# Performance work log

Hardware: AMD Instinct MI355X
Metric: run time of the kernel (lower is better)

Reference implementation:

```python
import jax, jax.numpy as jnp
import numpy as np

E = 128       # embed_size
H = 256       # hidden_size
Q = 256       # query_size
B = 256       # batch size
N_ENT = 200000
N_REL = 500
N_NODES = 100000   # existing (head) nodes
N_NEW = 50000      # new tail nodes (segment_sum size)
M = 200000         # edges


def setup_inputs() -> dict:
    key = jax.random.key(0)
    ks = jax.random.split(key, 32)
    s = 0.02
    inp = {
        'entity_emb':   jax.random.normal(ks[0], (N_ENT, E), jnp.float32),
        'relation_emb': jax.random.normal(ks[1], (N_REL, E), jnp.float32),
        'node_hidden':  jax.random.normal(ks[2], (N_NODES, H), jnp.float32),
        'query_repr':   jax.random.normal(ks[3], (B, Q), jnp.float32),
        # attention params (Ws_attn, Wr_attn, Wqr_attn, w_alpha)
        'Ws':  jax.random.normal(ks[4], (H, H), jnp.float32) * s,
        'Wr':  jax.random.normal(ks[5], (E, H), jnp.float32) * s,
        'Wqr': jax.random.normal(ks[6], (E, H), jnp.float32) * s,
        'bqr': jnp.zeros((H,), jnp.float32),
        'w_alpha': jax.random.normal(ks[7], (H, 1), jnp.float32) * s,
        'b_alpha': jnp.zeros((1,), jnp.float32),
        # GRUCell (input = 2E message, hidden = H), torch layout [3H, in]
        'W_ih': jax.random.normal(ks[8], (3 * H, 2 * E), jnp.float32) * s,
        'W_hh': jax.random.normal(ks[9], (3 * H, H), jnp.float32) * s,
        'b_ih': jnp.zeros((3 * H,), jnp.float32),
        'b_hh': jnp.zeros((3 * H,), jnp.float32),
        # We2h: entity embed -> initial hidden
        'We2h_W': jax.random.normal(ks[10], (E, H), jnp.float32) * s,
        'We2h_b': jnp.zeros((H,), jnp.float32),
        # candidate_layer: [2E + H] -> H (agent_num = 1)
        'cand_W': jax.random.normal(ks[11], (2 * E + H, H), jnp.float32) * s,
        'cand_b': jnp.zeros((H,), jnp.float32),
        # rank_layer: [H + Q] -> 1
        'rank_W': jax.random.normal(ks[12], (H + Q, 1), jnp.float32) * s,
        'rank_b': jnp.zeros((1,), jnp.float32),
        # LayerNorm
        'ln_g': jnp.ones((H,), jnp.float32),
        'ln_b': jnp.zeros((H,), jnp.float32),
        # edge list (int constants)
        'head_node':     jax.random.randint(ks[13], (M,), 0, N_NODES, jnp.int32),
        'edge_rel':      jax.random.randint(ks[14], (M,), 0, N_REL, jnp.int32),
        'tail_ent':      jax.random.randint(ks[15], (M,), 0, N_ENT, jnp.int32),
        'tail_node':     jax.random.randint(ks[16], (M,), 0, N_NEW, jnp.int32),
        'query_rel':     jax.random.randint(ks[17], (M,), 0, N_REL, jnp.int32),
        'batch_idx':     jax.random.randint(ks[18], (M,), 0, B, jnp.int32),
        'tail_node_ent': jax.random.randint(ks[19], (N_NEW,), 0, N_ENT, jnp.int32),
    }
    return inp


def reference(entity_emb, relation_emb, node_hidden, query_repr,
              Ws, Wr, Wqr, bqr, w_alpha, b_alpha,
              W_ih, W_hh, b_ih, b_hh, We2h_W, We2h_b,
              cand_W, cand_b, rank_W, rank_b, ln_g, ln_b,
              head_node, edge_rel, tail_ent, tail_node, query_rel,
              batch_idx, tail_node_ent):
    lrelu = lambda x: jax.nn.leaky_relu(x, 0.01)
    # --- per-edge attention: w_alpha(ReLU(Ws h_s + Wr h_r + Wqr h_q)) ---
    hs = node_hidden[head_node]            # [M, H]
    hr = relation_emb[edge_rel]            # [M, E]
    hq = relation_emb[query_rel]           # [M, E]
    attn_feat = jax.nn.relu(hs @ Ws + hr @ Wr + hq @ Wqr + bqr)   # [M, H]
    alpha = jax.nn.sigmoid(attn_feat @ w_alpha + b_alpha)         # [M, 1]
    # --- attention-weighted message (rel || tail entity) scattered to tails ---
    te = entity_emb[tail_ent]                                     # [M, E]
    msg = jnp.concatenate([hr, te], axis=-1) * alpha              # [M, 2E]
    agg = jax.ops.segment_sum(msg, tail_node, num_segments=N_NEW) # [N_NEW, 2E]
    # --- GRUCell update of tail-node hidden states ---
    h_prev = lrelu(entity_emb[tail_node_ent] @ We2h_W + We2h_b)   # [N_NEW, H]
    gx = agg @ W_ih.T + b_ih                                      # [N_NEW, 3H]
    gh = h_prev @ W_hh.T + b_hh
    xr, xz, xn = jnp.split(gx, 3, axis=-1)
    hr_, hz_, hn_ = jnp.split(gh, 3, axis=-1)
    r = jax.nn.sigmoid(xr + hr_)
    z = jax.nn.sigmoid(xz + hz_)
    n = jnp.tanh(xn + r * hn_)
    h_new = (1.0 - z) * n + z * h_prev                            # [N_NEW, H]
    mu = jnp.mean(h_new, axis=-1, keepdims=True)
    var = jnp.var(h_new, axis=-1, keepdims=True)
    h_new = (h_new - mu) * jax.lax.rsqrt(var + 1e-5) * ln_g + ln_b
    # --- candidate scoring: candidate_layer + rank_layer ---
    cand_in = jnp.concatenate([te, hr, h_new[tail_node]], axis=-1)   # [M, 2E+H]
    cand_h = lrelu(cand_in @ cand_W + cand_b)                        # [M, H]
    rank_in = jnp.concatenate([cand_h, query_repr[batch_idx]], -1)   # [M, H+Q]
    scores = (rank_in @ rank_W + rank_b)[:, 0]                       # [M]
    return scores
```

## Files before the change

### kernel.cpp

```cpp
#include <hip/hip_runtime.h>
#include <math.h>


#define ACT_NONE 0
#define ACT_LRELU 1

typedef __attribute__((ext_vector_type(8))) short short8;
typedef __attribute__((ext_vector_type(4))) float floatx4;

__device__ __forceinline__ ushort f2b(float x) {
    union { float f; unsigned u; } v; v.f = x;
    return (ushort)((v.u + 0x7fffu + ((v.u >> 16) & 1u)) >> 16);
}
__device__ __forceinline__ float b2f(ushort b) {
    union { unsigned u; float f; } v; v.u = ((unsigned)b) << 16;
    return v.f;
}
__device__ __forceinline__ void gload16(const ushort* g, ushort* l) {
    __builtin_amdgcn_global_load_lds(
        (const __attribute__((address_space(1))) void*)g,
        (__attribute__((address_space(3))) void*)l, 16, 0, 0);
}

__global__ __launch_bounds__(256) void gemm_k(
    const float* __restrict__ A, const float* __restrict__ B,
    const float* __restrict__ bias, float* __restrict__ C,
    int M, int N, int K, const int* __restrict__ a_idx, int act)
{
    __shared__ float As[16][68];
    __shared__ float Bs[16][68];
    const int tid = threadIdx.x;
    const int tx = tid & 15, ty = tid >> 4;
    const int m0 = blockIdx.x * 64, n0 = blockIdx.y * 64;
    float acc[4][4] = {};
    const int ar  = tid >> 2;
    const int ac4 = (tid & 3) * 4;
    const int brow = tid >> 4;
    const int bc4  = (tid & 15) * 4;
    const int gm = m0 + ar;
    const float* Arow = nullptr;
    if (gm < M) {
        int r = a_idx ? a_idx[gm] : gm;
        Arow = A + (size_t)r * K;
    }
    for (int k0 = 0; k0 < K; k0 += 16) {
        float4 av = make_float4(0.f, 0.f, 0.f, 0.f);
        if (Arow) av = *(const float4*)(Arow + k0 + ac4);
        As[ac4 + 0][ar] = av.x;
        As[ac4 + 1][ar] = av.y;
        As[ac4 + 2][ar] = av.z;
        As[ac4 + 3][ar] = av.w;
        float4 bv = *(const float4*)(B + (size_t)(k0 + brow) * N + n0 + bc4);
        *(float4*)&Bs[brow][bc4] = bv;
        __syncthreads();
        #pragma unroll
        for (int kk = 0; kk < 16; ++kk) {
            float4 a4 = *(float4*)&As[kk][ty << 2];
            float4 b4 = *(float4*)&Bs[kk][tx << 2];
            float avr[4] = {a4.x, a4.y, a4.z, a4.w};
            float bvr[4] = {b4.x, b4.y, b4.z, b4.w};
            #pragma unroll
            for (int i = 0; i < 4; ++i)
                #pragma unroll
                for (int j = 0; j < 4; ++j)
                    acc[i][j] = fmaf(avr[i], bvr[j], acc[i][j]);
        }
        __syncthreads();
    }
    const int n = n0 + (tx << 2);
    float4 bv4 = make_float4(0.f, 0.f, 0.f, 0.f);
    if (bias) bv4 = *(const float4*)(bias + n);
    #pragma unroll
    for (int i = 0; i < 4; ++i) {
        int m = m0 + (ty << 2) + i;
        if (m >= M) continue;
        float v0 = acc[i][0] + bv4.x;
        float v1 = acc[i][1] + bv4.y;
        float v2 = acc[i][2] + bv4.z;
        float v3 = acc[i][3] + bv4.w;
        if (act == ACT_LRELU) {
            v0 = v0 > 0.f ? v0 : 0.01f * v0;
            v1 = v1 > 0.f ? v1 : 0.01f * v1;
            v2 = v2 > 0.f ? v2 : 0.01f * v2;
            v3 = v3 > 0.f ? v3 : 0.01f * v3;
        }
        *(float4*)(C + (size_t)m * N + n) = make_float4(v0, v1, v2, v3);
    }
}

__global__ __launch_bounds__(256) void convert16_k(
    const float* __restrict__ in, ushort* __restrict__ out, int n)
{
    int i = blockIdx.x * 256 + threadIdx.x;
    if (i < n) out[i] = f2b(in[i]);
}
__global__ __launch_bounds__(256) void transpose16_k(
    const float* __restrict__ in, ushort* __restrict__ out, int k0, int KS, int N)
{
    int i = blockIdx.x * 256 + threadIdx.x;
    if (i >= KS * N) return;
    int k = i / N, n = i - k * N;
    out[(size_t)n * KS + k] = f2b(in[(size_t)(k0 + k) * N + n]);
}

__global__ __launch_bounds__(256) void gemm16p_k(
    const ushort* __restrict__ A16, const int* __restrict__ a_idx,
    const ushort* __restrict__ BT, const float* __restrict__ bias,
    float* __restrict__ C, ushort* __restrict__ C16,
    int M, int N, int K, int act)
{
    __shared__ ushort As[2][128 * 32];
    __shared__ ushort Bs[2][128 * 32];
    const int tid = threadIdx.x;
    const int l = tid & 63, w = tid >> 6;
    const int m0 = blockIdx.y * 128, n0 = blockIdx.x * 128;

    const ushort* agp[2];
    const ushort* bgp[2];
    #pragma unroll
    for (int j = 0; j < 2; ++j) {
        int row = j * 64 + w * 16 + (l >> 2);
        int seg = (l & 3) ^ (row & 3);
        int r = m0 + row; if (r >= M) r = M - 1;
        int rr = a_idx ? a_idx[r] : r;
        agp[j] = A16 + (size_t)rr * K + seg * 8;
        bgp[j] = BT + (size_t)(n0 + row) * K + seg * 8;
    }

    const int wm = (w & 1) * 64, wn = (w >> 1) * 64;
    const int cl = l & 15, q = l >> 4;
    const int sseg = (q ^ (cl & 3)) * 8;
    const int aoff = (wm + cl) * 32 + sseg;
    const int boff = (wn + cl) * 32 + sseg;

    floatx4 acc[4][4];
    #pragma unroll
    for (int mi = 0; mi < 4; ++mi)
        #pragma unroll
        for (int ni = 0; ni < 4; ++ni) acc[mi][ni] = 0.f;

    const int NT = K >> 5;
    #pragma unroll
    for (int j = 0; j < 2; ++j) {
        gload16(agp[j], &As[0][j * 2048 + w * 512]);
        gload16(bgp[j], &Bs[0][j * 2048 + w * 512]);
    }
    __syncthreads();

    int buf = 0;
    for (int t = 0; t < NT; ++t) {
        if (t + 1 < NT) {
            int k0 = (t + 1) * 32;
            #pragma unroll
            for (int j = 0; j < 2; ++j) {
                gload16(agp[j] + k0, &As[buf ^ 1][j * 2048 + w * 512]);
                gload16(bgp[j] + k0, &Bs[buf ^ 1][j * 2048 + w * 512]);
            }
        }
        short8 af[4], bf[4];
        #pragma unroll
        for (int mi = 0; mi < 4; ++mi) af[mi] = *(short8*)&As[buf][aoff + mi * 512];
        #pragma unroll
        for (int ni = 0; ni < 4; ++ni) bf[ni] = *(short8*)&Bs[buf][boff + ni * 512];
        #pragma unroll
        for (int mi = 0; mi < 4; ++mi)
            #pragma unroll
            for (int ni = 0; ni < 4; ++ni)
                acc[mi][ni] = __builtin_amdgcn_mfma_f32_16x16x32_bf16(
                    bf[ni], af[mi], acc[mi][ni], 0, 0, 0);
        __syncthreads();
        buf ^= 1;
    }

    #pragma unroll
    for (int mi = 0; mi < 4; ++mi) {
        int row = m0 + wm + mi * 16 + cl;
        if (row >= M) continue;
        #pragma unroll
        for (int ni = 0; ni < 4; ++ni) {
            int col = n0 + wn + ni * 16 + q * 4;
            float4 bv = bias ? *(const float4*)(bias + col)
                             : make_float4(0.f, 0.f, 0.f, 0.f);
            float v[4];
            #pragma unroll
            for (int r = 0; r < 4; ++r) {
                float x = acc[mi][ni][r] + ((const float*)&bv)[r];
                if (act == ACT_LRELU) x = x > 0.f ? x : 0.01f * x;
                v[r] = x;
            }
            if (C16) {
                ushort4 u;
                u.x = f2b(v[0]); u.y = f2b(v[1]); u.z = f2b(v[2]); u.w = f2b(v[3]);
                *(ushort4*)(C16 + (size_t)row * N + col) = u;
            }
            if (C) *(float4*)(C + (size_t)row * N + col) =
                       make_float4(v[0], v[1], v[2], v[3]);
        }
    }
}

__global__ __launch_bounds__(256) void gemm16pf_k(
    const float* __restrict__ A, const ushort* __restrict__ BT,
    const float* __restrict__ bias, ushort* __restrict__ C16,
    int M, int N, int K, int act)
{
    __shared__ ushort As[2][128 * 32];
    __shared__ ushort Bs[2][128 * 32];
    const int tid = threadIdx.x;
    const int l = tid & 63, w = tid >> 6;
    const int m0 = blockIdx.y * 128, n0 = blockIdx.x * 128;

    const int rowbase = tid >> 3, f4 = tid & 7;
    const float* arow[4];
    int awadr[4];
    #pragma unroll
    for (int i = 0; i < 4; ++i) {
        int row = rowbase + i * 32;
        int r = m0 + row; if (r >= M) r = M - 1;
        arow[i] = A + (size_t)r * K;
        awadr[i] = row * 32 + (((f4 >> 1) ^ (row & 3)) * 8) + (f4 & 1) * 4;
    }
    const ushort* bgp[2];
    #pragma unroll
    for (int j = 0; j < 2; ++j) {
        int row = j * 64 + w * 16 + (l >> 2);
        int seg = (l & 3) ^ (row & 3);
        bgp[j] = BT + (size_t)(n0 + row) * K + seg * 8;
    }

    const int wm = (w & 1) * 64, wn = (w >> 1) * 64;
    const int cl = l & 15, q = l >> 4;
    const int sseg = (q ^ (cl & 3)) * 8;
    const int aoff = (wm + cl) * 32 + sseg;
    const int boff = (wn + cl) * 32 + sseg;

    floatx4 acc[4][4];
    #pragma unroll
    for (int mi = 0; mi < 4; ++mi)
        #pragma unroll
        for (int ni = 0; ni < 4; ++ni) acc[mi][ni] = 0.f;

    const int NT = K >> 5;
    #pragma unroll
    for (int j = 0; j < 2; ++j) gload16(bgp[j], &Bs[0][j * 2048 + w * 512]);
    #pragma unroll
    for (int i = 0; i < 4; ++i) {
        float4 v = *(const float4*)(arow[i] + f4 * 4);
        ushort4 u; u.x = f2b(v.x); u.y = f2b(v.y); u.z = f2b(v.z); u.w = f2b(v.w);
        *(ushort4*)&As[0][awadr[i]] = u;
    }
    __syncthreads();

    int buf = 0;
    for (int t = 0; t < NT; ++t) {
        float4 av[4];
        if (t + 1 < NT) {
            int k0 = (t + 1) * 32;
            #pragma unroll
            for (int j = 0; j < 2; ++j)
                gload16(bgp[j] + k0, &Bs[buf ^ 1][j * 2048 + w * 512]);
            #pragma unroll
            for (int i = 0; i < 4; ++i)
                av[i] = *(const float4*)(arow[i] + k0 + f4 * 4);
        }
        short8 af[4], bf[4];
        #pragma unroll
        for (int mi = 0; mi < 4; ++mi) af[mi] = *(short8*)&As[buf][aoff + mi * 512];
        #pragma unroll
        for (int ni = 0; ni < 4; ++ni) bf[ni] = *(short8*)&Bs[buf][boff + ni * 512];
        #pragma unroll
        for (int mi = 0; mi < 4; ++mi)
            #pragma unroll
            for (int ni = 0; ni < 4; ++ni)
                acc[mi][ni] = __builtin_amdgcn_mfma_f32_16x16x32_bf16(
                    bf[ni], af[mi], acc[mi][ni], 0, 0, 0);
        if (t + 1 < NT) {
            #pragma unroll
            for (int i = 0; i < 4; ++i) {
                ushort4 u;
                u.x = f2b(av[i].x); u.y = f2b(av[i].y);
                u.z = f2b(av[i].z); u.w = f2b(av[i].w);
                *(ushort4*)&As[buf ^ 1][awadr[i]] = u;
            }
        }
        __syncthreads();
        buf ^= 1;
    }

    #pragma unroll
    for (int mi = 0; mi < 4; ++mi) {
        int row = m0 + wm + mi * 16 + cl;
        if (row >= M) continue;
        #pragma unroll
        for (int ni = 0; ni < 4; ++ni) {
            int col = n0 + wn + ni * 16 + q * 4;
            float4 bv = bias ? *(const float4*)(bias + col)
                             : make_float4(0.f, 0.f, 0.f, 0.f);
            ushort4 u;
            float x0 = acc[mi][ni][0] + bv.x;
            float x1 = acc[mi][ni][1] + bv.y;
            float x2 = acc[mi][ni][2] + bv.z;
            float x3 = acc[mi][ni][3] + bv.w;
            if (act == ACT_LRELU) {
                x0 = x0 > 0.f ? x0 : 0.01f * x0;
                x1 = x1 > 0.f ? x1 : 0.01f * x1;
                x2 = x2 > 0.f ? x2 : 0.01f * x2;
                x3 = x3 > 0.f ? x3 : 0.01f * x3;
            }
            u.x = f2b(x0); u.y = f2b(x1); u.z = f2b(x2); u.w = f2b(x3);
            *(ushort4*)(C16 + (size_t)row * N + col) = u;
        }
    }
}

__global__ __launch_bounds__(256) void qdot_k(
    const float* __restrict__ q, const float* __restrict__ rank_W,
    float* __restrict__ qdot)
{
    int b = blockIdx.x * 4 + (threadIdx.x >> 6);
    int l = threadIdx.x & 63;
    float s = 0.f;
    #pragma unroll
    for (int k = 0; k < 4; ++k) {
        int h = l + k * 64;
        s += q[(size_t)b * 256 + h] * rank_W[256 + h];
    }
    #pragma unroll
    for (int off = 32; off; off >>= 1) s += __shfl_xor(s, off, 64);
    if (l == 0) qdot[b] = s;
}

__global__ __launch_bounds__(256) void alpha_k(
    const ushort* __restrict__ nodeWs16, const float* __restrict__ relWr,
    const float* __restrict__ relWqr, const float* __restrict__ bqr,
    const float* __restrict__ w_alpha, const float* __restrict__ b_alpha_p,
    const int* __restrict__ hcsr_hn, const int* __restrict__ hcsr_er,
    const int* __restrict__ hcsr_qr, const int* __restrict__ hcsr_e,
    float* __restrict__ alpha_out)
{
    const int tid = threadIdx.x;
    const int e0 = blockIdx.x * 32;
    __shared__ int hn[32], er[32], qr[32], se[32];
    if (tid < 32) {
        int i = e0 + tid;
        hn[tid] = hcsr_hn[i]; er[tid] = hcsr_er[i];
        qr[tid] = hcsr_qr[i]; se[tid] = hcsr_e[i];
    }
    __syncthreads();
    const int tx = tid & 63, ty = tid >> 6;
    const int c = tx * 4;
    const float4 bq = *(const float4*)(bqr + c);
    const float4 wa = *(const float4*)(w_alpha + c);
    float part[8];
    #pragma unroll
    for (int i2 = 0; i2 < 8; ++i2) {
        int i = ty * 8 + i2;
        ushort4 a16 = *(const ushort4*)(nodeWs16 + (size_t)hn[i] * 256 + c);
        float4 b = *(const float4*)(relWr + (size_t)er[i] * 256 + c);
        float4 d = *(const float4*)(relWqr + (size_t)qr[i] * 256 + c);
        float x0 = fmaxf(b2f(a16.x) + b.x + d.x + bq.x, 0.f);
        float x1 = fmaxf(b2f(a16.y) + b.y + d.y + bq.y, 0.f);
        float x2 = fmaxf(b2f(a16.z) + b.z + d.z + bq.z, 0.f);
        float x3 = fmaxf(b2f(a16.w) + b.w + d.w + bq.w, 0.f);
        part[i2] = x0 * wa.x + x1 * wa.y + x2 * wa.z + x3 * wa.w;
    }
    #pragma unroll
    for (int off = 32; off; off >>= 1)
        #pragma unroll
        for (int i2 = 0; i2 < 8; ++i2)
            part[i2] += __shfl_xor(part[i2], off, 64);
    if (tx == 0) {
        float ba = b_alpha_p[0];
        #pragma unroll
        for (int i2 = 0; i2 < 8; ++i2)
            alpha_out[se[ty * 8 + i2]] = 1.f / (1.f + __expf(-(part[i2] + ba)));
    }
}

__global__ __launch_bounds__(256) void hist_k(
    const int* __restrict__ key, int* __restrict__ deg, int M)
{
    int e = blockIdx.x * 256 + threadIdx.x;
    if (e < M) atomicAdd(&deg[key[e]], 1);
}
__global__ __launch_bounds__(512) void scan1_k(
    const int* __restrict__ deg, int* __restrict__ partial, int N)
{
    __shared__ int sm[512];
    int i = blockIdx.x * 512 + threadIdx.x;
    sm[threadIdx.x] = (i < N) ? deg[i] : 0;
    __syncthreads();
    for (int off = 256; off; off >>= 1) {
        if (threadIdx.x < off) sm[threadIdx.x] += sm[threadIdx.x + off];
        __syncthreads();
    }
    if (threadIdx.x == 0) partial[blockIdx.x] = sm[0];
}
__global__ __launch_bounds__(256) void scan2_k(
    int* __restrict__ partial, int nPart, int* __restrict__ offsets, int N, int M)
{
    __shared__ int sm[256];
    int t = threadIdx.x;
    int v = (t < nPart) ? partial[t] : 0;
    sm[t] = v;
    __syncthreads();
    for (int off = 1; off < 256; off <<= 1) {
        int add = (t >= off) ? sm[t - off] : 0;
        __syncthreads();
        sm[t] += add;
        __syncthreads();
    }
    if (t < nPart) partial[t] = sm[t] - v;
    if (t == 0) offsets[N] = M;
}
__global__ __launch_bounds__(512) void scan3_k(
    const int* __restrict__ deg, const int* __restrict__ partial,
    int* __restrict__ offsets, int* __restrict__ cursor, int N)
{
    __shared__ int sm[512];
    int i = blockIdx.x * 512 + threadIdx.x;
    int t = threadIdx.x;
    int v = (i < N) ? deg[i] : 0;
    sm[t] = v;
    __syncthreads();
    for (int off = 1; off < 512; off <<= 1) {
        int add = (t >= off) ? sm[t - off] : 0;
        __syncthreads();
        sm[t] += add;
        __syncthreads();
    }
    if (i < N) {
        int excl = partial[blockIdx.x] + sm[t] - v;
        offsets[i] = excl;
        cursor[i] = excl;
    }
}
__global__ __launch_bounds__(256) void fill_k(
    const int* __restrict__ tail_node, const int* __restrict__ tail_ent,
    const int* __restrict__ edge_rel, const int* __restrict__ batch_idx,
    int* __restrict__ cursor, int* __restrict__ ce, int* __restrict__ cte,
    int* __restrict__ cer, int* __restrict__ ctn, int* __restrict__ cbi, int M)
{
    int e = blockIdx.x * 256 + threadIdx.x;
    if (e < M) {
        int tn = tail_node[e];
        int pos = atomicAdd(&cursor[tn], 1);
        ce[pos] = e; cte[pos] = tail_ent[e]; cer[pos] = edge_rel[e];
        ctn[pos] = tn; cbi[pos] = batch_idx[e];
    }
}
__global__ __launch_bounds__(256) void hfill_k(
    const int* __restrict__ head_node, const int* __restrict__ edge_rel,
    const int* __restrict__ query_rel, int* __restrict__ cursor,
    int* __restrict__ hhn, int* __restrict__ her, int* __restrict__ hqr,
    int* __restrict__ he, int M)
{
    int e = blockIdx.x * 256 + threadIdx.x;
    if (e < M) {
        int h = head_node[e];
        int pos = atomicAdd(&cursor[h], 1);
        hhn[pos] = h; her[pos] = edge_rel[e]; hqr[pos] = query_rel[e]; he[pos] = e;
    }
}

__global__ __launch_bounds__(256) void agg_csr_k(
    const float* __restrict__ relation_emb, const ushort* __restrict__ ent16,
    const float* __restrict__ alpha, const int* __restrict__ csr_e,
    const int* __restrict__ csr_er, const int* __restrict__ csr_te,
    const int* __restrict__ offsets, ushort* __restrict__ agg16)
{
    int node = blockIdx.x * 4 + (threadIdx.x >> 6);
    int lane = threadIdx.x & 63;
    int beg = offsets[node], end = offsets[node + 1];
    float4 acc = make_float4(0.f, 0.f, 0.f, 0.f);
    const int c = lane * 4;
    for (int j = beg; j < end; ++j) {
        float a = alpha[csr_e[j]];
        float4 v;
        if (lane < 32) {
            v = *(const float4*)(relation_emb + (size_t)csr_er[j] * 128 + c);
        } else {
            ushort4 u = *(const ushort4*)(ent16 + (size_t)csr_te[j] * 128 + (c - 128));
            v = make_float4(b2f(u.x), b2f(u.y), b2f(u.z), b2f(u.w));
        }
        acc.x += v.x * a; acc.y += v.y * a;
        acc.z += v.z * a; acc.w += v.w * a;
    }
    ushort4 o;
    o.x = f2b(acc.x); o.y = f2b(acc.y); o.z = f2b(acc.z); o.w = f2b(acc.w);
    *(ushort4*)(agg16 + (size_t)node * 256 + c) = o;
}

__global__ __launch_bounds__(256) void gru_ln_k(
    const ushort* __restrict__ gx, const ushort* __restrict__ gh,
    const ushort* __restrict__ h_prev, const float* __restrict__ ln_g,
    const float* __restrict__ ln_b, ushort* __restrict__ h_new16, int n0)
{
    int nl = blockIdx.x * 4 + (threadIdx.x >> 6);
    int lane = threadIdx.x & 63;
    int n = n0 + nl;
    const ushort* gxr = gx + (size_t)nl * 768;
    const ushort* ghr = gh + (size_t)nl * 768;
    const ushort* hpr = h_prev + (size_t)n * 256;
    float hv[4]; float s = 0.f, s2 = 0.f;
    #pragma unroll
    for (int q2 = 0; q2 < 4; ++q2) {
        int h = lane + q2 * 64;
        float xr = b2f(gxr[h]), xz = b2f(gxr[256 + h]), xn = b2f(gxr[512 + h]);
        float hr_ = b2f(ghr[h]), hn_ = b2f(ghr[512 + h]);
        float hz_ = b2f(ghr[256 + h]);
        float hp = b2f(hpr[h]);
        float r = 1.f / (1.f + __expf(-(xr + hr_)));
        float z = 1.f / (1.f + __expf(-(xz + hz_)));
        float nn = tanhf(xn + r * hn_);
        float v = (1.f - z) * nn + z * hp;
        hv[q2] = v; s += v; s2 += v * v;
    }
    #pragma unroll
    for (int off = 32; off; off >>= 1) {
        s  += __shfl_xor(s, off, 64);
        s2 += __shfl_xor(s2, off, 64);
    }
    float mean = s * (1.f / 256.f);
    float var  = s2 * (1.f / 256.f) - mean * mean;
    float rstd = rsqrtf(var + 1e-5f);
    ushort* outr = h_new16 + (size_t)n * 256;
    #pragma unroll
    for (int q2 = 0; q2 < 4; ++q2) {
        int h = lane + q2 * 64;
        outr[h] = f2b((hv[q2] - mean) * rstd * ln_g[h] + ln_b[h]);
    }
}

__global__ __launch_bounds__(256) void score_mfma_k(
    const ushort* __restrict__ ent16, const ushort* __restrict__ candW1T,
    const ushort* __restrict__ relCand16, const ushort* __restrict__ hnewCand16,
    const float* __restrict__ rank_W, const float* __restrict__ rank_b_p,
    const float* __restrict__ qdot,
    const int* __restrict__ csr_e, const int* __restrict__ csr_te,
    const int* __restrict__ csr_er, const int* __restrict__ csr_tn,
    const int* __restrict__ csr_bi, float* __restrict__ scores, int M)
{
    __shared__ ushort As[128 * 136];
    __shared__ int s_er[128], s_tn[128];
    __shared__ float s_part[4][128];
    const int tid = threadIdx.x;
    const int e0 = blockIdx.x * 128;
    int cnt = M - e0; if (cnt > 128) cnt = 128;

    if (tid < 128) {
        int idx = e0 + (tid < cnt ? tid : 0);
        s_er[tid] = csr_er[idx];
        s_tn[tid] = csr_tn[idx];
    }
    {
        int row = tid >> 1;
        int idx = e0 + (row < cnt ? row : 0);
        const ushort* ar = ent16 + (size_t)csr_te[idx] * 128;
        int s0 = (tid & 1) * 8;
        #pragma unroll
        for (int j = 0; j < 8; ++j) {
            int seg = s0 + j;
            int slot = seg ^ (row & 3);
            *(uint4*)&As[row * 136 + slot * 8] = *(const uint4*)(ar + seg * 8);
        }
    }
    __syncthreads();

    const int l = tid & 63, w = tid >> 6;
    const int cl = l & 15, q = l >> 4;

    float rowsum[8];
    #pragma unroll
    for (int mi = 0; mi < 8; ++mi) rowsum[mi] = 0.f;

    #pragma unroll
    for (int ch = 0; ch < 2; ++ch) {
        floatx4 acc[8][2];
        #pragma unroll
        for (int mi = 0; mi < 8; ++mi)
            #pragma unroll
            for (int ni = 0; ni < 2; ++ni) acc[mi][ni] = 0.f;

        const ushort* bb = candW1T + (size_t)(w * 64 + ch * 32 + cl) * 128 + q * 8;
        #pragma unroll
        for (int k0 = 0; k0 < 128; k0 += 32) {
            short8 bf[2];
            #pragma unroll
            for (int ni = 0; ni < 2; ++ni)
                bf[ni] = *(const short8*)(bb + ni * 2048 + k0);
            #pragma unroll
            for (int mi = 0; mi < 8; ++mi) {
                int row = mi * 16 + cl;
                int slot = (((k0 >> 3) + q) ^ (cl & 3));
                short8 af = *(short8*)&As[row * 136 + slot * 8];
                #pragma unroll
                for (int ni = 0; ni < 2; ++ni)
                    acc[mi][ni] = __builtin_amdgcn_mfma_f32_16x16x32_bf16(
                        bf[ni], af, acc[mi][ni], 0, 0, 0);
            }
        }
        #pragma unroll
        for (int mi = 0; mi < 8; ++mi) {
            int row = mi * 16 + cl;
            int er = s_er[row], tn = s_tn[row];
            #pragma unroll
            for (int ni = 0; ni < 2; ++ni) {
                int col = w * 64 + ch * 32 + ni * 16 + q * 4;
                ushort4 rc = *(const ushort4*)(relCand16 + (size_t)er * 256 + col);
                ushort4 hc = *(const ushort4*)(hnewCand16 + (size_t)tn * 256 + col);
                float4 rw = *(const float4*)(rank_W + col);
                float v0 = acc[mi][ni][0] + b2f(rc.x) + b2f(hc.x);
                float v1 = acc[mi][ni][1] + b2f(rc.y) + b2f(hc.y);
                float v2 = acc[mi][ni][2] + b2f(rc.z) + b2f(hc.z);
                float v3 = acc[mi][ni][3] + b2f(rc.w) + b2f(hc.w);
                v0 = v0 > 0.f ? v0 : 0.01f * v0;
                v1 = v1 > 0.f ? v1 : 0.01f * v1;
                v2 = v2 > 0.f ? v2 : 0.01f * v2;
                v3 = v3 > 0.f ? v3 : 0.01f * v3;
                rowsum[mi] += v0 * rw.x + v1 * rw.y + v2 * rw.z + v3 * rw.w;
            }
        }
    }
    #pragma unroll
    for (int mi = 0; mi < 8; ++mi) {
        rowsum[mi] += __shfl_xor(rowsum[mi], 16, 64);
        rowsum[mi] += __shfl_xor(rowsum[mi], 32, 64);
    }
    if (q == 0) {
        #pragma unroll
        for (int mi = 0; mi < 8; ++mi)
            s_part[w][mi * 16 + cl] = rowsum[mi];
    }
    __syncthreads();
    if (tid < cnt) {
        int idx = e0 + tid;
        float s = s_part[0][tid] + s_part[1][tid] + s_part[2][tid] + s_part[3][tid]
                + qdot[csr_bi[idx]] + rank_b_p[0];
        scores[csr_e[idx]] = s;
    }
}

extern "C" void kernel_launch(void* const* d_in, const int* in_sizes, int n_in,
                              void* d_out, int out_size, void* d_ws, size_t ws_size,
                              hipStream_t stream)
{
    const float* entity_emb   = (const float*)d_in[0];
    const float* relation_emb = (const float*)d_in[1];
    const float* node_hidden  = (const float*)d_in[2];
    const float* query_repr   = (const float*)d_in[3];
    const float* Ws    = (const float*)d_in[4];
    const float* Wr    = (const float*)d_in[5];
    const float* Wqr   = (const float*)d_in[6];
    const float* bqr   = (const float*)d_in[7];
    const float* w_alpha = (const float*)d_in[8];
    const float* b_alpha = (const float*)d_in[9];
    const float* W_ih  = (const float*)d_in[10];
    const float* W_hh  = (const float*)d_in[11];
    const float* b_ih  = (const float*)d_in[12];
    const float* b_hh  = (const float*)d_in[13];
    const float* We2h_W = (const float*)d_in[14];
    const float* We2h_b = (const float*)d_in[15];
    const float* cand_W = (const float*)d_in[16];
    const float* cand_b = (const float*)d_in[17];
    const float* rank_W = (const float*)d_in[18];
    const float* rank_b = (const float*)d_in[19];
    const float* ln_g  = (const float*)d_in[20];
    const float* ln_b  = (const float*)d_in[21];
    const int* head_node = (const int*)d_in[22];
    const int* edge_rel  = (const int*)d_in[23];
    const int* tail_ent  = (const int*)d_in[24];
    const int* tail_node = (const int*)d_in[25];
    const int* query_rel = (const int*)d_in[26];
    const int* batch_idx = (const int*)d_in[27];
    const int* tail_node_ent = (const int*)d_in[28];
    float* out = (float*)d_out;
    (void)in_sizes; (void)n_in; (void)out_size; (void)ws_size;

    const int M = 200000, NNEW = 50000, NNODES = 100000, NREL = 500;
    const int NENT = 200000, E = 128;
    const int NCHUNK = 4, NC = NNEW / NCHUNK;
    const int NP_T = (NNEW + 511) / 512;
    const int NP_H = (NNODES + 511) / 512;

    float* w = (float*)d_ws;
    float* relWr    = w; w += NREL * 256;
    float* relWqr   = w; w += NREL * 256;
    float* relCand  = w; w += NREL * 256;
    float* qdot     = w; w += 256;
    float* alpha    = w; w += M;
    ushort* h_prev16   = (ushort*)w; w += (size_t)NNEW * 256 / 2;
    ushort* agg16      = (ushort*)w; w += (size_t)NNEW * 256 / 2;
    ushort* hnewCand16 = (ushort*)w; w += (size_t)NNEW * 256 / 2;
    ushort* relCand16  = (ushort*)w; w += (NREL * 256) / 2;
    ushort* ent16      = (ushort*)w; w += (size_t)NENT * E / 2;
    ushort* h_new16    = (ushort*)w; w += (size_t)NNEW * 256 / 2;
    ushort* W_ih16    = (ushort*)w; w += (768 * 256) / 2;
    ushort* W_hh16    = (ushort*)w; w += (768 * 256) / 2;
    ushort* WsT16     = (ushort*)w; w += (256 * 256) / 2;
    ushort* We2hT16   = (ushort*)w; w += (256 * 128) / 2;
    ushort* candW1T16 = (ushort*)w; w += (256 * 128) / 2;
    ushort* candW3T16 = (ushort*)w; w += (256 * 256) / 2;
    int* deg      = (int*)w; w += NNEW;
    int* offsets  = (int*)w; w += NNEW + 1;
    int* cursor   = (int*)w; w += NNEW;
    int* deg2     = (int*)w; w += NNODES;
    int* offsets2 = (int*)w; w += NNODES + 1;
    int* cursor2  = (int*)w; w += NNODES;
    int* partial  = (int*)w; w += 512;
    int* csr_e  = (int*)w; w += M;
    int* csr_te = (int*)w; w += M;
    int* csr_er = (int*)w; w += M;
    int* csr_tn = (int*)w; w += M;
    int* csr_bi = (int*)w; w += M;
    int* hcsr_hn = (int*)w; w += M;
    int* hcsr_er = (int*)w; w += M;
    int* hcsr_qr = (int*)w; w += M;
    int* hcsr_e  = (int*)w; w += M;
    w = (float*)(((uintptr_t)w + 63) & ~(uintptr_t)63);
    float* big = w;
    ushort* nodeWs16 = (ushort*)big;
    ushort* gx16 = (ushort*)big;
    ushort* gh16 = (ushort*)big + (size_t)NC * 768;

    hipMemsetAsync(deg, 0, NNEW * sizeof(int), stream);
    hipMemsetAsync(deg2, 0, NNODES * sizeof(int), stream);
    hist_k<<<(M + 255) / 256, 256, 0, stream>>>(tail_node, deg, M);
    scan1_k<<<NP_T, 512, 0, stream>>>(deg, partial, NNEW);
    scan2_k<<<1, 256, 0, stream>>>(partial, NP_T, offsets, NNEW, M);
    scan3_k<<<NP_T, 512, 0, stream>>>(deg, partial, offsets, cursor, NNEW);
    fill_k<<<(M + 255) / 256, 256, 0, stream>>>(tail_node, tail_ent, edge_rel,
        batch_idx, cursor, csr_e, csr_te, csr_er, csr_tn, csr_bi, M);
    hist_k<<<(M + 255) / 256, 256, 0, stream>>>(head_node, deg2, M);
    scan1_k<<<NP_H, 512, 0, stream>>>(deg2, partial, NNODES);
    scan2_k<<<1, 256, 0, stream>>>(partial, NP_H, offsets2, NNODES, M);
    scan3_k<<<NP_H, 512, 0, stream>>>(deg2, partial, offsets2, cursor2, NNODES);
    hfill_k<<<(M + 255) / 256, 256, 0, stream>>>(head_node, edge_rel, query_rel,
        cursor2, hcsr_hn, hcsr_er, hcsr_qr, hcsr_e, M);

    convert16_k<<<(NENT * E + 255) / 256, 256, 0, stream>>>(entity_emb, ent16, NENT * E);
    convert16_k<<<768, 256, 0, stream>>>(W_ih, W_ih16, 768 * 256);
    convert16_k<<<768, 256, 0, stream>>>(W_hh, W_hh16, 768 * 256);
    transpose16_k<<<256, 256, 0, stream>>>(Ws, WsT16, 0, 256, 256);
    transpose16_k<<<128, 256, 0, stream>>>(We2h_W, We2hT16, 0, 128, 256);
    transpose16_k<<<128, 256, 0, stream>>>(cand_W, candW1T16, 0, 128, 256);
    transpose16_k<<<256, 256, 0, stream>>>(cand_W, candW3T16, 256, 256, 256);
    gemm_k<<<dim3(8, 4), 256, 0, stream>>>(relation_emb, Wr,  nullptr, relWr,  NREL, 256, 128, nullptr, ACT_NONE);
    gemm_k<<<dim3(8, 4), 256, 0, stream>>>(relation_emb, Wqr, nullptr, relWqr, NREL, 256, 128, nullptr, ACT_NONE);
    gemm_k<<<dim3(8, 4), 256, 0, stream>>>(relation_emb, cand_W + 128 * 256, nullptr, relCand, NREL, 256, 128, nullptr, ACT_NONE);
    convert16_k<<<(NREL * 256 + 255) / 256, 256, 0, stream>>>(relCand, relCand16, NREL * 256);
    qdot_k<<<64, 256, 0, stream>>>(query_repr, rank_W, qdot);

    gemm16pf_k<<<dim3(2, (NNODES + 127) / 128), 256, 0, stream>>>(
        node_hidden, WsT16, nullptr, nodeWs16, NNODES, 256, 256, ACT_NONE);

    alpha_k<<<M / 32, 256, 0, stream>>>(nodeWs16, relWr, relWqr, bqr, w_alpha, b_alpha,
                                        hcsr_hn, hcsr_er, hcsr_qr, hcsr_e, alpha);

    agg_csr_k<<<NNEW / 4, 256, 0, stream>>>(relation_emb, ent16, alpha,
                                            csr_e, csr_er, csr_te, offsets, agg16);

    gemm16p_k<<<dim3(2, (NNEW + 127) / 128), 256, 0, stream>>>(
        ent16, tail_node_ent, We2hT16, We2h_b, nullptr, h_prev16, NNEW, 256, 128, ACT_LRELU);

    for (int ch = 0; ch < NCHUNK; ++ch) {
        int n0 = ch * NC;
        gemm16p_k<<<dim3(6, (NC + 127) / 128), 256, 0, stream>>>(
            agg16 + (size_t)n0 * 256, nullptr, W_ih16, b_ih, nullptr, gx16, NC, 768, 256, ACT_NONE);
        gemm16p_k<<<dim3(6, (NC + 127) / 128), 256, 0, stream>>>(
            h_prev16 + (size_t)n0 * 256, nullptr, W_hh16, b_hh, nullptr, gh16, NC, 768, 256, ACT_NONE);
        gru_ln_k<<<NC / 4, 256, 0, stream>>>(gx16, gh16, h_prev16, ln_g, ln_b, h_new16, n0);
    }

    gemm16p_k<<<dim3(2, (NNEW + 127) / 128), 256, 0, stream>>>(
        h_new16, nullptr, candW3T16, cand_b, nullptr, hnewCand16, NNEW, 256, 256, ACT_NONE);

    score_mfma_k<<<(M + 127) / 128, 256, 0, stream>>>(
        ent16, candW1T16, relCand16, hnewCand16, rank_W, rank_b, qdot,
        csr_e, csr_te, csr_er, csr_tn, csr_bi, out, M);
}
```

Measured before the change: 883.6 us.

## Retile node-hidden GEMM to full-width tiles and restructure score kernel staging

The fp32-input node_hidden x Ws GEMM now uses 64x256 tiles, so each block covers all 256 output columns and reads each row of node_hidden once instead of twice across two column blocks. The score kernel gathers entity rows into LDS with async global_load_lds in an MFMA-friendly swizzled layout. It also iterates four 16-column chunks with a single B fragment per k-step to reduce register pressure, with launch bounds raised to request 4 blocks per CU. In exchange, the GEMM's B tile in LDS grows and per-block A reuse shrinks, and the score kernel loads rank_W less often but does more chunk iterations.

Measured after the change: 1.004 ms. 1.14x slower.

```diff
diff --git a/kernel.cpp b/kernel.cpp
--- a/kernel.cpp
+++ b/kernel.cpp
@@ -199,40 +199,33 @@
     }
 }
 
-__global__ __launch_bounds__(256) void gemm16pf_k(
+__global__ __launch_bounds__(256) void gemm16pw_k(
     const float* __restrict__ A, const ushort* __restrict__ BT,
     const float* __restrict__ bias, ushort* __restrict__ C16,
-    int M, int N, int K, int act)
-{
-    __shared__ ushort As[2][128 * 32];
-    __shared__ ushort Bs[2][128 * 32];
+    int M, int K, int act)
+{
+    __shared__ ushort As[2][64 * 36];
+    __shared__ ushort Bs[2][256 * 32];
     const int tid = threadIdx.x;
     const int l = tid & 63, w = tid >> 6;
-    const int m0 = blockIdx.y * 128, n0 = blockIdx.x * 128;
-
-    const int rowbase = tid >> 3, f4 = tid & 7;
-    const float* arow[4];
-    int awadr[4];
-    #pragma unroll
-    for (int i = 0; i < 4; ++i) {
-        int row = rowbase + i * 32;
-        int r = m0 + row; if (r >= M) r = M - 1;
-        arow[i] = A + (size_t)r * K;
-        awadr[i] = row * 32 + (((f4 >> 1) ^ (row & 3)) * 8) + (f4 & 1) * 4;
-    }
-    const ushort* bgp[2];
-    #pragma unroll
-    for (int j = 0; j < 2; ++j) {
+    const int m0 = blockIdx.x * 64;
+
+    const int ar = tid >> 2, af4 = tid & 3;
+    int rr = m0 + ar; if (rr >= M) rr = M - 1;
+    const float* agp = A + (size_t)rr * K + af4 * 8;
+    const int awadr = ar * 36 + af4 * 8;
+
+    const ushort* bgp[4];
+    #pragma unroll
+    for (int j = 0; j < 4; ++j) {
         int row = j * 64 + w * 16 + (l >> 2);
         int seg = (l & 3) ^ (row & 3);
-        bgp[j] = BT + (size_t)(n0 + row) * K + seg * 8;
-    }
-
-    const int wm = (w & 1) * 64, wn = (w >> 1) * 64;
+        bgp[j] = BT + (size_t)row * K + seg * 8;
+    }
+
     const int cl = l & 15, q = l >> 4;
-    const int sseg = (q ^ (cl & 3)) * 8;
-    const int aoff = (wm + cl) * 32 + sseg;
-    const int boff = (wn + cl) * 32 + sseg;
+    const int aoff = cl * 36 + q * 8;
+    const int boff = (w * 64 + cl) * 32 + (q ^ (cl & 3)) * 8;
 
     floatx4 acc[4][4];
     #pragma unroll
@@ -242,46 +235,47 @@
 
     const int NT = K >> 5;
     #pragma unroll
-    for (int j = 0; j < 2; ++j) gload16(bgp[j], &Bs[0][j * 2048 + w * 512]);
-    #pragma unroll
-    for (int i = 0; i < 4; ++i) {
-        float4 v = *(const float4*)(arow[i] + f4 * 4);
-        ushort4 u; u.x = f2b(v.x); u.y = f2b(v.y); u.z = f2b(v.z); u.w = f2b(v.w);
-        *(ushort4*)&As[0][awadr[i]] = u;
+    for (int j = 0; j < 4; ++j)
+        gload16(bgp[j], &Bs[0][j * 2048 + w * 512]);
+    {
+        float4 v0 = *(const float4*)(agp);
+        float4 v1 = *(const float4*)(agp + 4);
+        ushort4 u0, u1;
+        u0.x = f2b(v0.x); u0.y = f2b(v0.y); u0.z = f2b(v0.z); u0.w = f2b(v0.w);
+        u1.x = f2b(v1.x); u1.y = f2b(v1.y); u1.z = f2b(v1.z); u1.w = f2b(v1.w);
+        *(ushort4*)&As[0][awadr] = u0;
+        *(ushort4*)&As[0][awadr + 4] = u1;
     }
     __syncthreads();
 
     int buf = 0;
     for (int t = 0; t < NT; ++t) {
-        float4 av[4];
+        float4 v0, v1;
         if (t + 1 < NT) {
             int k0 = (t + 1) * 32;
             #pragma unroll
-            for (int j = 0; j < 2; ++j)
+            for (int j = 0; j < 4; ++j)
                 gload16(bgp[j] + k0, &Bs[buf ^ 1][j * 2048 + w * 512]);
-            #pragma unroll
-            for (int i = 0; i < 4; ++i)
-                av[i] = *(const float4*)(arow[i] + k0 + f4 * 4);
-        }
-        short8 af[4], bf[4];
-        #pragma unroll
-        for (int mi = 0; mi < 4; ++mi) af[mi] = *(short8*)&As[buf][aoff + mi * 512];
+            v0 = *(const float4*)(agp + k0);
+            v1 = *(const float4*)(agp + k0 + 4);
+        }
+        short8 bf[4];
         #pragma unroll
         for (int ni = 0; ni < 4; ++ni) bf[ni] = *(short8*)&Bs[buf][boff + ni * 512];
         #pragma unroll
-        for (int mi = 0; mi < 4; ++mi)
+        for (int mi = 0; mi < 4; ++mi) {
+            short8 af = *(short8*)&As[buf][aoff + mi * 576];
             #pragma unroll
             for (int ni = 0; ni < 4; ++ni)
                 acc[mi][ni] = __builtin_amdgcn_mfma_f32_16x16x32_bf16(
-                    bf[ni], af[mi], acc[mi][ni], 0, 0, 0);
+                    bf[ni], af, acc[mi][ni], 0, 0, 0);
+        }
         if (t + 1 < NT) {
-            #pragma unroll
-            for (int i = 0; i < 4; ++i) {
-                ushort4 u;
-                u.x = f2b(av[i].x); u.y = f2b(av[i].y);
-                u.z = f2b(av[i].z); u.w = f2b(av[i].w);
-                *(ushort4*)&As[buf ^ 1][awadr[i]] = u;
-            }
+            ushort4 u0, u1;
+            u0.x = f2b(v0.x); u0.y = f2b(v0.y); u0.z = f2b(v0.z); u0.w = f2b(v0.w);
+            u1.x = f2b(v1.x); u1.y = f2b(v1.y); u1.z = f2b(v1.z); u1.w = f2b(v1.w);
+            *(ushort4*)&As[buf ^ 1][awadr] = u0;
+            *(ushort4*)&As[buf ^ 1][awadr + 4] = u1;
         }
         __syncthreads();
         buf ^= 1;
@@ -289,11 +283,11 @@
 
     #pragma unroll
     for (int mi = 0; mi < 4; ++mi) {
-        int row = m0 + wm + mi * 16 + cl;
+        int row = m0 + mi * 16 + cl;
         if (row >= M) continue;
         #pragma unroll
         for (int ni = 0; ni < 4; ++ni) {
-            int col = n0 + wn + ni * 16 + q * 4;
+            int col = w * 64 + ni * 16 + q * 4;
             float4 bv = bias ? *(const float4*)(bias + col)
                              : make_float4(0.f, 0.f, 0.f, 0.f);
             ushort4 u;
@@ -308,7 +302,7 @@
                 x3 = x3 > 0.f ? x3 : 0.01f * x3;
             }
             u.x = f2b(x0); u.y = f2b(x1); u.z = f2b(x2); u.w = f2b(x3);
-            *(ushort4*)(C16 + (size_t)row * N + col) = u;
+            *(ushort4*)(C16 + (size_t)row * 256 + col) = u;
         }
     }
 }
@@ -532,7 +526,7 @@
     }
 }
 
-__global__ __launch_bounds__(256) void score_mfma_k(
+__global__ __launch_bounds__(256, 4) void score_mfma_k(
     const ushort* __restrict__ ent16, const ushort* __restrict__ candW1T,
     const ushort* __restrict__ relCand16, const ushort* __restrict__ hnewCand16,
     const float* __restrict__ rank_W, const float* __restrict__ rank_b_p,
@@ -541,85 +535,77 @@
     const int* __restrict__ csr_er, const int* __restrict__ csr_tn,
     const int* __restrict__ csr_bi, float* __restrict__ scores, int M)
 {
-    __shared__ ushort As[128 * 136];
-    __shared__ int s_er[128], s_tn[128];
+    __shared__ ushort As[128 * 128];
+    __shared__ int s_te[128], s_er[128], s_tn[128];
     __shared__ float s_part[4][128];
     const int tid = threadIdx.x;
+    const int l = tid & 63, w = tid >> 6;
     const int e0 = blockIdx.x * 128;
     int cnt = M - e0; if (cnt > 128) cnt = 128;
 
     if (tid < 128) {
         int idx = e0 + (tid < cnt ? tid : 0);
+        s_te[tid] = csr_te[idx];
         s_er[tid] = csr_er[idx];
         s_tn[tid] = csr_tn[idx];
     }
+    __syncthreads();
+
     {
-        int row = tid >> 1;
-        int idx = e0 + (row < cnt ? row : 0);
-        const ushort* ar = ent16 + (size_t)csr_te[idx] * 128;
-        int s0 = (tid & 1) * 8;
+        const int lr = l >> 2, ls = l & 3;
         #pragma unroll
         for (int j = 0; j < 8; ++j) {
-            int seg = s0 + j;
-            int slot = seg ^ (row & 3);
-            *(uint4*)&As[row * 136 + slot * 8] = *(const uint4*)(ar + seg * 8);
-        }
-    }
-    __syncthreads();
-
-    const int l = tid & 63, w = tid >> 6;
+            int c = w * 8 + j;
+            int kt = c >> 3;
+            int row = (c & 7) * 16 + lr;
+            int sg = kt * 4 + (ls ^ (row & 3));
+            gload16(ent16 + (size_t)s_te[row] * 128 + sg * 8, &As[c * 512]);
+        }
+    }
+    __syncthreads();
+
     const int cl = l & 15, q = l >> 4;
+    const int sslot = (q ^ (cl & 3)) * 8;
 
     float rowsum[8];
     #pragma unroll
     for (int mi = 0; mi < 8; ++mi) rowsum[mi] = 0.f;
 
     #pragma unroll
-    for (int ch = 0; ch < 2; ++ch) {
-        floatx4 acc[8][2];
-        #pragma unroll
-        for (int mi = 0; mi < 8; ++mi)
-            #pragma unroll
-            for (int ni = 0; ni < 2; ++ni) acc[mi][ni] = 0.f;
-
-        const ushort* bb = candW1T + (size_t)(w * 64 + ch * 32 + cl) * 128 + q * 8;
-        #pragma unroll
-        for (int k0 = 0; k0 < 128; k0 += 32) {
-            short8 bf[2];
-            #pragma unroll
-            for (int ni = 0; ni < 2; ++ni)
-                bf[ni] = *(const short8*)(bb + ni * 2048 + k0);
+    for (int ch = 0; ch < 4; ++ch) {
+        floatx4 acc[8];
+        #pragma unroll
+        for (int mi = 0; mi < 8; ++mi) acc[mi] = 0.f;
+
+        const ushort* bb = candW1T + (size_t)(w * 64 + ch * 16 + cl) * 128 + q * 8;
+        #pragma unroll
+        for (int kt = 0; kt < 4; ++kt) {
+            short8 bf = *(const short8*)(bb + kt * 32);
+            const int abase = kt * 4096 + cl * 32 + sslot;
             #pragma unroll
             for (int mi = 0; mi < 8; ++mi) {
-                int row = mi * 16 + cl;
-                int slot = (((k0 >> 3) + q) ^ (cl & 3));
-                short8 af = *(short8*)&As[row * 136 + slot * 8];
-                #pragma unroll
-                for (int ni = 0; ni < 2; ++ni)
-                    acc[mi][ni] = __builtin_amdgcn_mfma_f32_16x16x32_bf16(
-                        bf[ni], af, acc[mi][ni], 0, 0, 0);
+                short8 af = *(short8*)&As[abase + mi * 512];
+                acc[mi] = __builtin_amdgcn_mfma_f32_16x16x32_bf16(
+                    bf, af, acc[mi], 0, 0, 0);
             }
         }
+        const int col = w * 64 + ch * 16 + q * 4;
+        const float4 rw = *(const float4*)(rank_W + col);
         #pragma unroll
         for (int mi = 0; mi < 8; ++mi) {
             int row = mi * 16 + cl;
             int er = s_er[row], tn = s_tn[row];
-            #pragma unroll
-            for (int ni = 0; ni < 2; ++ni) {
-                int col = w * 64 + ch * 32 + ni * 16 + q * 4;
-                ushort4 rc = *(const ushort4*)(relCand16 + (size_t)er * 256 + col);
-                ushort4 hc = *(const ushort4*)(hnewCand16 + (size_t)tn * 256 + col);
-                float4 rw = *(const float4*)(rank_W + col);
-                float v0 = acc[mi][ni][0] + b2f(rc.x) + b2f(hc.x);
-                float v1 = acc[mi][ni][1] + b2f(rc.y) + b2f(hc.y);
-                float v2 = acc[mi][ni][2] + b2f(rc.z) + b2f(hc.z);
-                float v3 = acc[mi][ni][3] + b2f(rc.w) + b2f(hc.w);
-                v0 = v0 > 0.f ? v0 : 0.01f * v0;
-                v1 = v1 > 0.f ? v1 : 0.01f * v1;
-                v2 = v2 > 0.f ? v2 : 0.01f * v2;
-                v3 = v3 > 0.f ? v3 : 0.01f * v3;
-                rowsum[mi] += v0 * rw.x + v1 * rw.y + v2 * rw.z + v3 * rw.w;
-            }
+            ushort4 rc = *(const ushort4*)(relCand16 + (size_t)er * 256 + col);
+            ushort4 hc = *(const ushort4*)(hnewCand16 + (size_t)tn * 256 + col);
+            float v0 = acc[mi][0] + b2f(rc.x) + b2f(hc.x);
+            float v1 = acc[mi][1] + b2f(rc.y) + b2f(hc.y);
+            float v2 = acc[mi][2] + b2f(rc.z) + b2f(hc.z);
+            float v3 = acc[mi][3] + b2f(rc.w) + b2f(hc.w);
+            v0 = v0 > 0.f ? v0 : 0.01f * v0;
+            v1 = v1 > 0.f ? v1 : 0.01f * v1;
+            v2 = v2 > 0.f ? v2 : 0.01f * v2;
+            v3 = v3 > 0.f ? v3 : 0.01f * v3;
+            rowsum[mi] += v0 * rw.x + v1 * rw.y + v2 * rw.z + v3 * rw.w;
         }
     }
     #pragma unroll
@@ -751,8 +737,8 @@
     convert16_k<<<(NREL * 256 + 255) / 256, 256, 0, stream>>>(relCand, relCand16, NREL * 256);
     qdot_k<<<64, 256, 0, stream>>>(query_repr, rank_W, qdot);
 
-    gemm16pf_k<<<dim3(2, (NNODES + 127) / 128), 256, 0, stream>>>(
-        node_hidden, WsT16, nullptr, nodeWs16, NNODES, 256, 256, ACT_NONE);
+    gemm16pw_k<<<(NNODES + 63) / 64, 256, 0, stream>>>(
+        node_hidden, WsT16, nullptr, nodeWs16, NNODES, 256, ACT_NONE);
 
     alpha_k<<<M / 32, 256, 0, stream>>>(nodeWs16, relWr, relWqr, bqr, w_alpha, b_alpha,
                                         hcsr_hn, hcsr_er, hcsr_qr, hcsr_e, alpha);
```
